# Optimization experiments

Measured on AMD Instinct MI355X. Metric: run time of the kernel, lower is better.

The kernel has to match this reference:

```python
import jax, jax.numpy as jnp
import numpy as np

E = 200000  # num edges == num nodes (x is built as ones((edge_index.size(1), D)))
D = 128     # embedding_dim
R = 4       # number of relation types
NEG_SLOPE = 0.01


def _xavier(key, shape):
    fan_in, fan_out = shape[-2], shape[-1]
    limit = np.sqrt(6.0 / (fan_in + fan_out)).astype(np.float32)
    return jax.random.uniform(key, shape, jnp.float32, -limit, limit)


def setup_inputs() -> dict:
    key = jax.random.key(0)
    ks = jax.random.split(key, 8)
    edge_index = jax.random.randint(ks[0], (2, E), 0, E)
    edge_type = jax.random.randint(ks[1], (E,), 0, R)
    edge_attr = jax.random.uniform(ks[2], (E,), dtype=jnp.float32)
    return {
        "edge_index": edge_index,
        "edge_type": edge_type,
        "edge_attr": edge_attr,
        "weights1": _xavier(ks[3], (R, D, D)), "bias1": jnp.zeros((D,), jnp.float32),
        "weights2": _xavier(ks[4], (R, D, D)), "bias2": jnp.zeros((D,), jnp.float32),
        "weights3": _xavier(ks[5], (R, D, D)), "bias3": jnp.zeros((D,), jnp.float32),
    }


def _conv(x, w, b, row, col, edge_type, edge_attr):
    # symmetric degree norm on target index (col), as in the torch code
    deg = jax.ops.segment_sum(jnp.ones((E,), x.dtype), col, num_segments=E)
    # deg**-0.5 with inf masked to 0 (isolated nodes) to keep the baseline finite
    dinv = jnp.where(deg > 0, jax.lax.rsqrt(jnp.where(deg > 0, deg, 1.0)), 0.0)
    norm = dinv[row] * dinv[col]                      # [E]
    xr = x[row]                                       # gather source nodes [E,D]
    # per-edge relation-indexed matmul: 4 dense GEMMs + select (avoids [E,D,D])
    msg = jnp.zeros((E, D), x.dtype)
    for r in range(R):
        msg = msg + jnp.where((edge_type == r)[:, None], xr @ w[r], 0.0)
    msg = msg * (edge_attr * norm)[:, None]
    out = jax.ops.segment_sum(msg, col, num_segments=E) + b  # scatter-add + bias
    return jax.nn.leaky_relu(out, NEG_SLOPE)          # dropout skipped (eval mode)


def reference(edge_index, edge_type, edge_attr,
              weights1, bias1, weights2, bias2, weights3, bias3):
    row, col = edge_index[0], edge_index[1]
    x = jnp.ones((E, D), jnp.float32)
    z1 = _conv(x, weights1, bias1, row, col, edge_type, edge_attr)
    z2 = _conv(z1, weights2, bias2, row, col, edge_type, edge_attr)
    z3 = _conv(z2, weights3, bias3, row, col, edge_type, edge_attr)
    return (x + z1 + z2 + z3) / 4.0
```

## Files before the change

kernel.cpp:

```cpp
#include <hip/hip_runtime.h>
#include <math.h>

constexpr int EN = 200000;
constexpr int D  = 128;
constexpr int R  = 4;
constexpr float NEG = 0.01f;

constexpr int NBLKE = (EN + 255) / 256;
constexpr int NPREP = 66;
constexpr int NCH   = (EN + 1023) / 1024;

static inline int ceil_div(int a, int b) { return (a + b - 1) / b; }

typedef __attribute__((ext_vector_type(8))) __bf16 bf16x8;
typedef __attribute__((ext_vector_type(4))) float f32x4;

__device__ __forceinline__ unsigned short f2bf(float f) {
    union { float f; unsigned u; } v; v.f = f;
    unsigned u = v.u + 0x7fffu + ((v.u >> 16) & 1u);
    return (unsigned short)(u >> 16);
}
__device__ __forceinline__ unsigned pack2bf(float a, float b) {
    return (unsigned)f2bf(a) | ((unsigned)f2bf(b) << 16);
}
__device__ __forceinline__ float bflo(unsigned m) { return __uint_as_float(m << 16); }
__device__ __forceinline__ float bfhi(unsigned m) { return __uint_as_float(m & 0xffff0000u); }

__device__ __forceinline__ void wswz_one(const float* __restrict__ w,
                                         unsigned short* __restrict__ wsw, int t) {
    int lane = t & 63, mt = (t >> 6) & 7, s = (t >> 9) & 3, r = t >> 11;
    int q = lane >> 4, n = mt * 16 + (lane & 15);
    union { unsigned short us[8]; uint4 u4; } o;
    #pragma unroll
    for (int j = 0; j < 8; ++j) {
        int k = s * 32 + q * 8 + j;
        o.us[j] = f2bf(w[((size_t)r * D + k) * D + n]);
    }
    *(uint4*)(wsw + (size_t)t * 8) = o.u4;
}

__global__ void k_cntprep(const int* __restrict__ col, const int* __restrict__ etyp,
                          const float* __restrict__ w1, const float* __restrict__ w2,
                          const float* __restrict__ w3,
                          int* __restrict__ cnt, int* __restrict__ rcnt,
                          unsigned short* __restrict__ w2b, unsigned short* __restrict__ w3b,
                          float* __restrict__ s1) {
    const int b = blockIdx.x, t = threadIdx.x;
    if (b < NBLKE) {
        __shared__ int lr[R];
        if (t < R) lr[t] = 0;
        __syncthreads();
        int e = b * 256 + t;
        if (e < EN) {
            atomicAdd(&cnt[col[e]], 1);
            atomicAdd(&lr[etyp[e]], 1);
        }
        __syncthreads();
        if (t < R && lr[t]) atomicAdd(&rcnt[t], lr[t]);
    } else {
        int g = (b - NBLKE) * 256 + t;
        if (g < 8192) {
            wswz_one(w2, w2b, g);
        } else if (g < 16384) {
            wswz_one(w3, w3b, g - 8192);
        } else if (g < 16896) {
            int t2 = g - 16384;
            int r = t2 >> 7, j = t2 & (D - 1);
            float s = 0.f;
            for (int k = 0; k < D; ++k) s += w1[((r << 7) + k) * D + j];
            s1[t2] = s;
        }
    }
}

__global__ void k_scanA(const int* __restrict__ cnt, int* __restrict__ part,
                        float* __restrict__ dinv) {
    __shared__ int sm[256];
    int t = threadIdx.x;
    int base = blockIdx.x * 1024 + t * 4;
    int s = 0;
    #pragma unroll
    for (int i = 0; i < 4; ++i) {
        int idx = base + i;
        if (idx < EN) {
            int v = cnt[idx];
            s += v;
            dinv[idx] = (v > 0) ? rsqrtf((float)v) : 0.f;
        }
    }
    sm[t] = s; __syncthreads();
    for (int off = 128; off > 0; off >>= 1) {
        if (t < off) sm[t] += sm[t + off];
        __syncthreads();
    }
    if (t == 0) part[blockIdx.x] = sm[0];
}

__global__ void k_scanB(const int* __restrict__ cnt, const int* __restrict__ part,
                        const int* __restrict__ rcnt,
                        int* __restrict__ rbase, int* __restrict__ cursor,
                        int* __restrict__ col_start, int* __restrict__ ccur,
                        int4* __restrict__ bk_pack) {
    __shared__ int sm[256];
    __shared__ int sbase[R + 1];
    __shared__ int scnt[R];
    int t = threadIdx.x, bid = blockIdx.x;
    sm[t] = (t < NCH) ? part[t] : 0;
    __syncthreads();
    for (int off = 1; off < 256; off <<= 1) {
        int u = 0; if (t >= off) u = sm[t - off];
        __syncthreads(); sm[t] += u; __syncthreads();
    }
    const int base0 = (bid > 0) ? sm[bid - 1] : 0;
    __syncthreads();
    int base = bid * 1024 + t * 4;
    int v[4]; int s = 0;
    #pragma unroll
    for (int i = 0; i < 4; ++i) { int idx = base + i; v[i] = (idx < EN) ? cnt[idx] : 0; s += v[i]; }
    sm[t] = s; __syncthreads();
    for (int off = 1; off < 256; off <<= 1) {
        int u = 0; if (t >= off) u = sm[t - off];
        __syncthreads(); sm[t] += u; __syncthreads();
    }
    int ex = ((t > 0) ? sm[t - 1] : 0) + base0;
    #pragma unroll
    for (int i = 0; i < 4; ++i) {
        int idx = base + i;
        if (idx < EN) { col_start[idx] = ex; ex += v[i]; ccur[idx] = 0; }
    }
    if (bid == 0) {
        if (t == 0) {
            int acc = 0;
            for (int r = 0; r < R; ++r) {
                sbase[r] = acc; rbase[r] = acc; cursor[r] = acc;
                int c0 = rcnt[r]; scnt[r] = c0;
                acc += (c0 + 15) & ~15;
            }
            sbase[R] = acc; rbase[R] = acc;
            col_start[EN] = EN;
        }
        __syncthreads();
        for (int r = 0; r < R; ++r) {
            int ps = sbase[r] + scnt[r], pe = sbase[r + 1];
            for (int i = ps + t; i < pe; i += 256)
                bk_pack[i] = make_int4(0, EN, 0, 0);
        }
    }
}

__global__ void k_bucket(const int* __restrict__ row, const int* __restrict__ col,
                         const int* __restrict__ etype, const float* __restrict__ attr,
                         const float* __restrict__ dinv, const int* __restrict__ col_start,
                         int* __restrict__ cursor, int* __restrict__ ccur,
                         int4* __restrict__ bk_pack, float* __restrict__ crel) {
    __shared__ int lcnt[R];
    __shared__ int lbase[R];
    int t = threadIdx.x;
    if (t < R) lcnt[t] = 0;
    __syncthreads();
    int e = blockIdx.x * 256 + t;
    int r = 0, rank = 0, c = 0, rw = 0;
    float cf = 0.f;
    if (e < EN) {
        r = etype[e];
        rank = atomicAdd(&lcnt[r], 1);
        c = col[e]; rw = row[e];
        cf = attr[e] * dinv[rw] * dinv[c];
    }
    __syncthreads();
    if (t < R) lbase[t] = lcnt[t] ? atomicAdd(&cursor[t], lcnt[t]) : 0;
    __syncthreads();
    if (e < EN) {
        int pos = lbase[r] + rank;
        int sp = col_start[c] + atomicAdd(&ccur[c], 1);
        bk_pack[pos] = make_int4(rw, sp, __float_as_int(cf), 0);
        atomicAdd(&crel[c * 4 + r], cf);
    }
}

template<bool ONFLY>
__global__ __launch_bounds__(256)
void k_gemm(const unsigned short* __restrict__ xb, const unsigned short* __restrict__ wsw,
            const int4* __restrict__ bk_pack, const int* __restrict__ rbase,
            const float* __restrict__ crel, const float* __restrict__ s1g,
            const float* __restrict__ b1,
            unsigned short* __restrict__ msgb) {
    const int t = threadIdx.x;
    __shared__ unsigned short xpose[4][16 * 144];
    __shared__ float ls1[R * D];
    __shared__ float lb1[D];
    if constexpr (ONFLY) {
        ls1[t] = s1g[t];
        ls1[t + 256] = s1g[t + 256];
        if (t < D) lb1[t] = b1[t];
        __syncthreads();
    }
    const int tile = blockIdx.x * 4 + (t >> 6);
    const int e16 = tile * 16;
    if (e16 >= rbase[R]) return;
    const int r = (e16 >= rbase[1]) + (e16 >= rbase[2]) + (e16 >= rbase[3]);
    const int l = t & 63, q = l >> 4, n16 = l & 15;
    const int p = e16 + n16;
    const int4 bk = bk_pack[p];
    const int srow = bk.x;
    const int dp = bk.y;
    const float cf = __int_as_float(bk.z);

    bf16x8 xf[4];
    if constexpr (ONFLY) {
        const float4 cr = ((const float4*)crel)[srow];
        #pragma unroll
        for (int s = 0; s < 4; ++s) {
            union { unsigned short us[8]; bf16x8 v; } o;
            #pragma unroll
            for (int j = 0; j < 8; ++j) {
                int k = s * 32 + q * 8 + j;
                float xv = lb1[k] + cr.x * ls1[k] + cr.y * ls1[D + k]
                         + cr.z * ls1[2 * D + k] + cr.w * ls1[3 * D + k];
                xv = (xv > 0.f) ? xv : NEG * xv;
                o.us[j] = f2bf(xv);
            }
            xf[s] = o.v;
        }
    } else {
        const unsigned short* xrow = xb + (size_t)srow * D;
        #pragma unroll
        for (int s = 0; s < 4; ++s)
            xf[s] = *(const bf16x8*)(xrow + s * 32 + q * 8);
    }

    const unsigned short* wr = wsw + ((size_t)r * 2048 + l) * 8;

    f32x4 acc[8];
    #pragma unroll
    for (int mt = 0; mt < 8; ++mt) acc[mt] = (f32x4){0.f, 0.f, 0.f, 0.f};

    #pragma unroll
    for (int s = 0; s < 4; ++s) {
        #pragma unroll
        for (int mt = 0; mt < 8; ++mt) {
            bf16x8 wf = *(const bf16x8*)(wr + (size_t)(s * 512 + mt * 64) * 8);
            acc[mt] = __builtin_amdgcn_mfma_f32_16x16x32_bf16(wf, xf[s], acc[mt], 0, 0, 0);
        }
    }

    unsigned short* lbuf = xpose[t >> 6];
    #pragma unroll
    for (int mt = 0; mt < 8; ++mt) {
        uint2 u;
        u.x = pack2bf(acc[mt].x * cf, acc[mt].y * cf);
        u.y = pack2bf(acc[mt].z * cf, acc[mt].w * cf);
        *(uint2*)&lbuf[n16 * 144 + mt * 16 + q * 4] = u;
    }
    #pragma unroll
    for (int ro = 0; ro < 4; ++ro) {
        int e = ro * 4 + q;
        uint4 v = *(const uint4*)&lbuf[e * 144 + n16 * 8];
        int rdp = __shfl(dp, e);
        *(uint4*)(msgb + (size_t)rdp * D + n16 * 8) = v;
    }
}

__global__ void k_agg(const unsigned* __restrict__ msgb32, const float* __restrict__ bias,
                      const int* __restrict__ col_start,
                      unsigned* __restrict__ z2out,
                      const float* __restrict__ crel, const float* __restrict__ s1g,
                      const float* __restrict__ b1, const unsigned* __restrict__ z2in,
                      float* __restrict__ dout, int mode) {
    __shared__ float lb[D];
    __shared__ float ls1[R * D];
    __shared__ float lb1[D];
    int t = threadIdx.x;
    if (t < D) lb[t] = bias[t];
    if (mode == 3) {
        ls1[t] = s1g[t];
        ls1[t + 256] = s1g[t + 256];
        if (t < D) lb1[t] = b1[t];
    }
    __syncthreads();
    int lane = t & 63;
    for (int c = blockIdx.x * 4 + (t >> 6); c < EN; c += gridDim.x * 4) {
        int st = col_start[c], pe = col_start[c + 1];
        float a0 = 0.f, a1 = 0.f;
        for (int p = st; p < pe; ++p) {
            unsigned m = msgb32[(size_t)p * 64 + lane];
            a0 += bflo(m); a1 += bfhi(m);
        }
        a0 += lb[lane * 2]; a1 += lb[lane * 2 + 1];
        a0 = (a0 > 0.f) ? a0 : NEG * a0;
        a1 = (a1 > 0.f) ? a1 : NEG * a1;
        size_t ix = (size_t)c * 64 + lane;
        if (mode == 2) {
            z2out[ix] = pack2bf(a0, a1);
        } else {
            float4 cr = ((const float4*)crel)[c];
            int d0 = lane * 2, d1 = d0 + 1;
            float z1a = lb1[d0] + cr.x * ls1[d0] + cr.y * ls1[D + d0]
                      + cr.z * ls1[2 * D + d0] + cr.w * ls1[3 * D + d0];
            float z1b = lb1[d1] + cr.x * ls1[d1] + cr.y * ls1[D + d1]
                      + cr.z * ls1[2 * D + d1] + cr.w * ls1[3 * D + d1];
            z1a = (z1a > 0.f) ? z1a : NEG * z1a;
            z1b = (z1b > 0.f) ? z1b : NEG * z1b;
            unsigned u2 = z2in[ix];
            float2 o;
            o.x = (1.f + z1a + bflo(u2) + a0) * 0.25f;
            o.y = (1.f + z1b + bfhi(u2) + a1) * 0.25f;
            ((float2*)(dout + (size_t)c * D))[lane] = o;
        }
    }
}

extern "C" void kernel_launch(void* const* d_in, const int* in_sizes, int n_in,
                              void* d_out, int out_size, void* d_ws, size_t ws_size,
                              hipStream_t stream) {
    const int*   eidx = (const int*)d_in[0];
    const int*   row  = eidx;
    const int*   col  = eidx + EN;
    const int*   etyp = (const int*)d_in[1];
    const float* attr = (const float*)d_in[2];
    const float* w1   = (const float*)d_in[3];
    const float* b1   = (const float*)d_in[4];
    const float* w2   = (const float*)d_in[5];
    const float* b2   = (const float*)d_in[6];
    const float* w3   = (const float*)d_in[7];
    const float* b3   = (const float*)d_in[8];
    float* dout = (float*)d_out;

    char* wsb = (char*)d_ws;
    size_t off = 0;
    unsigned short* msgb = (unsigned short*)(wsb + off); off += (size_t)(EN + 1) * D * 2 + 512;
    unsigned short* xb2  = (unsigned short*)(wsb + off); off += (size_t)EN * D * 2;
    int*   col_start = (int*)(wsb + off); off += 800032;
    int*   cnt       = (int*)(wsb + off); off += (size_t)EN * 4;
    int*   rcnt      = (int*)(wsb + off); off += 16;
    float* crel      = (float*)(wsb + off); off += (size_t)EN * 16;
    int4*  bk_pack   = (int4*)(wsb + off); off += (size_t)(EN + 64) * 16;
    float* dinv      = (float*)(wsb + off); off += (size_t)EN * 4;
    unsigned short* w2b = (unsigned short*)(wsb + off); off += 131072;
    unsigned short* w3b = (unsigned short*)(wsb + off); off += 131072;
    int*   part      = (int*)(wsb + off); off += 1024;
    int*   rbase     = (int*)(wsb + off); off += 32;
    int*   cursor    = (int*)(wsb + off); off += 16;
    float* s1        = (float*)(wsb + off); off += (size_t)R * D * 4;
    int*   ccur      = (int*)msgb;

    dim3 blk(256);

    hipMemsetAsync(cnt, 0, (size_t)EN * 4 + 16 + (size_t)EN * 16, stream);
    k_cntprep<<<NBLKE + NPREP, blk, 0, stream>>>(col, etyp, w1, w2, w3,
                                                 cnt, rcnt, w2b, w3b, s1);
    k_scanA<<<NCH, blk, 0, stream>>>(cnt, part, dinv);
    k_scanB<<<NCH, blk, 0, stream>>>(cnt, part, rcnt, rbase, cursor, col_start,
                                     ccur, bk_pack);
    k_bucket<<<NBLKE, blk, 0, stream>>>(row, col, etyp, attr, dinv, col_start,
                                        cursor, ccur, bk_pack, crel);

    const int nTiles = ceil_div(EN + 64, 16);
    const int gB = ceil_div(nTiles, 4);
    k_gemm<true><<<gB, blk, 0, stream>>>(nullptr, w2b, bk_pack, rbase,
                                         crel, s1, b1, msgb);
    k_agg<<<2048, blk, 0, stream>>>((const unsigned*)msgb, b2, col_start,
                                    (unsigned*)xb2, crel, s1, b1, nullptr,
                                    nullptr, 2);
    k_gemm<false><<<gB, blk, 0, stream>>>(xb2, w3b, bk_pack, rbase,
                                          crel, s1, b1, msgb);
    k_agg<<<2048, blk, 0, stream>>>((const unsigned*)msgb, b3, col_start,
                                    nullptr, crel, s1, b1, (const unsigned*)xb2,
                                    dout, 3);
}
```

Measured before the change: 285.6 us.

## Fuse layer-2 aggregation into layer-3 GEMM gather and merge final aggregations

Drops the standalone layer-2 aggregation kernel. The layer-3 GEMM now rebuilds each source node's z2 on the fly by summing that node's incoming layer-2 messages, adding the bias and applying leaky ReLU before the MFMA. The final kernel sums both the layer-2 and layer-3 message buffers to produce z2 and z3 together, so the z2 buffer is never written out. This saves one launch and the z2 write and read, but each GEMM edge now re-reads the whole incoming-message segment of its source node, a redundant gather of about one average degree per edge. It also holds 32 extra float registers per lane and needs a second message buffer in the workspace.

```diff
diff --git a/kernel.cpp b/kernel.cpp
--- a/kernel.cpp
+++ b/kernel.cpp
@@ -178,23 +178,27 @@
     }
 }
 
-template<bool ONFLY>
+template<int LAYER>
 __global__ __launch_bounds__(256)
-void k_gemm(const unsigned short* __restrict__ xb, const unsigned short* __restrict__ wsw,
+void k_gemm(const unsigned short* __restrict__ msrc,
+            const unsigned short* __restrict__ wsw,
             const int4* __restrict__ bk_pack, const int* __restrict__ rbase,
+            const int* __restrict__ col_start,
             const float* __restrict__ crel, const float* __restrict__ s1g,
-            const float* __restrict__ b1,
-            unsigned short* __restrict__ msgb) {
+            const float* __restrict__ b1, const float* __restrict__ b2,
+            unsigned short* __restrict__ mdst) {
     const int t = threadIdx.x;
     __shared__ unsigned short xpose[4][16 * 144];
     __shared__ float ls1[R * D];
-    __shared__ float lb1[D];
-    if constexpr (ONFLY) {
+    __shared__ float lb[D];
+    if constexpr (LAYER == 2) {
         ls1[t] = s1g[t];
         ls1[t + 256] = s1g[t + 256];
-        if (t < D) lb1[t] = b1[t];
-        __syncthreads();
-    }
+        if (t < D) lb[t] = b1[t];
+    } else {
+        if (t < D) lb[t] = b2[t];
+    }
+    __syncthreads();
     const int tile = blockIdx.x * 4 + (t >> 6);
     const int e16 = tile * 16;
     if (e16 >= rbase[R]) return;
@@ -207,7 +211,7 @@
     const float cf = __int_as_float(bk.z);
 
     bf16x8 xf[4];
-    if constexpr (ONFLY) {
+    if constexpr (LAYER == 2) {
         const float4 cr = ((const float4*)crel)[srow];
         #pragma unroll
         for (int s = 0; s < 4; ++s) {
@@ -215,7 +219,7 @@
             #pragma unroll
             for (int j = 0; j < 8; ++j) {
                 int k = s * 32 + q * 8 + j;
-                float xv = lb1[k] + cr.x * ls1[k] + cr.y * ls1[D + k]
+                float xv = lb[k] + cr.x * ls1[k] + cr.y * ls1[D + k]
                          + cr.z * ls1[2 * D + k] + cr.w * ls1[3 * D + k];
                 xv = (xv > 0.f) ? xv : NEG * xv;
                 o.us[j] = f2bf(xv);
@@ -223,10 +227,32 @@
             xf[s] = o.v;
         }
     } else {
-        const unsigned short* xrow = xb + (size_t)srow * D;
+        const int st = col_start[srow], en = col_start[srow + 1];
+        float za[32];
         #pragma unroll
-        for (int s = 0; s < 4; ++s)
-            xf[s] = *(const bf16x8*)(xrow + s * 32 + q * 8);
+        for (int i = 0; i < 32; ++i) za[i] = 0.f;
+        for (int p2 = st; p2 < en; ++p2) {
+            const unsigned short* mrow = msrc + (size_t)p2 * D + q * 8;
+            #pragma unroll
+            for (int s = 0; s < 4; ++s) {
+                uint4 u = *(const uint4*)(mrow + s * 32);
+                za[s * 8 + 0] += bflo(u.x); za[s * 8 + 1] += bfhi(u.x);
+                za[s * 8 + 2] += bflo(u.y); za[s * 8 + 3] += bfhi(u.y);
+                za[s * 8 + 4] += bflo(u.z); za[s * 8 + 5] += bfhi(u.z);
+                za[s * 8 + 6] += bflo(u.w); za[s * 8 + 7] += bfhi(u.w);
+            }
+        }
+        #pragma unroll
+        for (int s = 0; s < 4; ++s) {
+            union { unsigned short us[8]; bf16x8 v; } o;
+            #pragma unroll
+            for (int j = 0; j < 8; ++j) {
+                float xv = za[s * 8 + j] + lb[s * 32 + q * 8 + j];
+                xv = (xv > 0.f) ? xv : NEG * xv;
+                o.us[j] = f2bf(xv);
+            }
+            xf[s] = o.v;
+        }
     }
 
     const unsigned short* wr = wsw + ((size_t)r * 2048 + l) * 8;
@@ -257,56 +283,50 @@
         int e = ro * 4 + q;
         uint4 v = *(const uint4*)&lbuf[e * 144 + n16 * 8];
         int rdp = __shfl(dp, e);
-        *(uint4*)(msgb + (size_t)rdp * D + n16 * 8) = v;
-    }
-}
-
-__global__ void k_agg(const unsigned* __restrict__ msgb32, const float* __restrict__ bias,
-                      const int* __restrict__ col_start,
-                      unsigned* __restrict__ z2out,
-                      const float* __restrict__ crel, const float* __restrict__ s1g,
-                      const float* __restrict__ b1, const unsigned* __restrict__ z2in,
-                      float* __restrict__ dout, int mode) {
-    __shared__ float lb[D];
+        *(uint4*)(mdst + (size_t)rdp * D + n16 * 8) = v;
+    }
+}
+
+__global__ void k_agg3(const unsigned* __restrict__ m2, const unsigned* __restrict__ m3,
+                       const float* __restrict__ b2v, const float* __restrict__ b3v,
+                       const int* __restrict__ col_start,
+                       const float* __restrict__ crel, const float* __restrict__ s1g,
+                       const float* __restrict__ b1, float* __restrict__ dout) {
     __shared__ float ls1[R * D];
-    __shared__ float lb1[D];
+    __shared__ float lb1[D], lb2[D], lb3[D];
     int t = threadIdx.x;
-    if (t < D) lb[t] = bias[t];
-    if (mode == 3) {
-        ls1[t] = s1g[t];
-        ls1[t + 256] = s1g[t + 256];
-        if (t < D) lb1[t] = b1[t];
-    }
+    ls1[t] = s1g[t];
+    ls1[t + 256] = s1g[t + 256];
+    if (t < D) { lb1[t] = b1[t]; lb2[t] = b2v[t]; lb3[t] = b3v[t]; }
     __syncthreads();
     int lane = t & 63;
     for (int c = blockIdx.x * 4 + (t >> 6); c < EN; c += gridDim.x * 4) {
         int st = col_start[c], pe = col_start[c + 1];
-        float a0 = 0.f, a1 = 0.f;
+        float s20 = 0.f, s21 = 0.f, s30 = 0.f, s31 = 0.f;
         for (int p = st; p < pe; ++p) {
-            unsigned m = msgb32[(size_t)p * 64 + lane];
-            a0 += bflo(m); a1 += bfhi(m);
-        }
-        a0 += lb[lane * 2]; a1 += lb[lane * 2 + 1];
-        a0 = (a0 > 0.f) ? a0 : NEG * a0;
-        a1 = (a1 > 0.f) ? a1 : NEG * a1;
-        size_t ix = (size_t)c * 64 + lane;
-        if (mode == 2) {
-            z2out[ix] = pack2bf(a0, a1);
-        } else {
-            float4 cr = ((const float4*)crel)[c];
-            int d0 = lane * 2, d1 = d0 + 1;
-            float z1a = lb1[d0] + cr.x * ls1[d0] + cr.y * ls1[D + d0]
-                      + cr.z * ls1[2 * D + d0] + cr.w * ls1[3 * D + d0];
-            float z1b = lb1[d1] + cr.x * ls1[d1] + cr.y * ls1[D + d1]
-                      + cr.z * ls1[2 * D + d1] + cr.w * ls1[3 * D + d1];
-            z1a = (z1a > 0.f) ? z1a : NEG * z1a;
-            z1b = (z1b > 0.f) ? z1b : NEG * z1b;
-            unsigned u2 = z2in[ix];
-            float2 o;
-            o.x = (1.f + z1a + bflo(u2) + a0) * 0.25f;
-            o.y = (1.f + z1b + bfhi(u2) + a1) * 0.25f;
-            ((float2*)(dout + (size_t)c * D))[lane] = o;
-        }
+            unsigned u2 = m2[(size_t)p * 64 + lane];
+            unsigned u3 = m3[(size_t)p * 64 + lane];
+            s20 += bflo(u2); s21 += bfhi(u2);
+            s30 += bflo(u3); s31 += bfhi(u3);
+        }
+        int d0 = lane * 2, d1 = d0 + 1;
+        float z2a = s20 + lb2[d0], z2b = s21 + lb2[d1];
+        z2a = (z2a > 0.f) ? z2a : NEG * z2a;
+        z2b = (z2b > 0.f) ? z2b : NEG * z2b;
+        float z3a = s30 + lb3[d0], z3b = s31 + lb3[d1];
+        z3a = (z3a > 0.f) ? z3a : NEG * z3a;
+        z3b = (z3b > 0.f) ? z3b : NEG * z3b;
+        float4 cr = ((const float4*)crel)[c];
+        float z1a = lb1[d0] + cr.x * ls1[d0] + cr.y * ls1[D + d0]
+                  + cr.z * ls1[2 * D + d0] + cr.w * ls1[3 * D + d0];
+        float z1b = lb1[d1] + cr.x * ls1[d1] + cr.y * ls1[D + d1]
+                  + cr.z * ls1[2 * D + d1] + cr.w * ls1[3 * D + d1];
+        z1a = (z1a > 0.f) ? z1a : NEG * z1a;
+        z1b = (z1b > 0.f) ? z1b : NEG * z1b;
+        float2 o;
+        o.x = (1.f + z1a + z2a + z3a) * 0.25f;
+        o.y = (1.f + z1b + z2b + z3b) * 0.25f;
+        ((float2*)(dout + (size_t)c * D))[lane] = o;
     }
 }
 
@@ -328,8 +348,8 @@
 
     char* wsb = (char*)d_ws;
     size_t off = 0;
-    unsigned short* msgb = (unsigned short*)(wsb + off); off += (size_t)(EN + 1) * D * 2 + 512;
-    unsigned short* xb2  = (unsigned short*)(wsb + off); off += (size_t)EN * D * 2;
+    unsigned short* msg2 = (unsigned short*)(wsb + off); off += (size_t)(EN + 1) * D * 2 + 512;
+    unsigned short* msg3 = (unsigned short*)(wsb + off); off += (size_t)(EN + 1) * D * 2 + 512;
     int*   col_start = (int*)(wsb + off); off += 800032;
     int*   cnt       = (int*)(wsb + off); off += (size_t)EN * 4;
     int*   rcnt      = (int*)(wsb + off); off += 16;
@@ -342,7 +362,7 @@
     int*   rbase     = (int*)(wsb + off); off += 32;
     int*   cursor    = (int*)(wsb + off); off += 16;
     float* s1        = (float*)(wsb + off); off += (size_t)R * D * 4;
-    int*   ccur      = (int*)msgb;
+    int*   ccur      = (int*)msg2;
 
     dim3 blk(256);
 
@@ -357,14 +377,10 @@
 
     const int nTiles = ceil_div(EN + 64, 16);
     const int gB = ceil_div(nTiles, 4);
-    k_gemm<true><<<gB, blk, 0, stream>>>(nullptr, w2b, bk_pack, rbase,
-                                         crel, s1, b1, msgb);
-    k_agg<<<2048, blk, 0, stream>>>((const unsigned*)msgb, b2, col_start,
-                                    (unsigned*)xb2, crel, s1, b1, nullptr,
-                                    nullptr, 2);
-    k_gemm<false><<<gB, blk, 0, stream>>>(xb2, w3b, bk_pack, rbase,
-                                          crel, s1, b1, msgb);
-    k_agg<<<2048, blk, 0, stream>>>((const unsigned*)msgb, b3, col_start,
-                                    nullptr, crel, s1, b1, (const unsigned*)xb2,
-                                    dout, 3);
-}
+    k_gemm<2><<<gB, blk, 0, stream>>>(nullptr, w2b, bk_pack, rbase, col_start,
+                                      crel, s1, b1, b2, msg2);
+    k_gemm<3><<<gB, blk, 0, stream>>>(msg2, w3b, bk_pack, rbase, col_start,
+                                      crel, s1, b1, b2, msg3);
+    k_agg3<<<2048, blk, 0, stream>>>((const unsigned*)msg2, (const unsigned*)msg3,
+                                     b2, b3, col_start, crel, s1, b1, dout);
+}
```

Result: faster. 263.6 us, median of 2 (-7.7%).
